# Kernel optimization log

Hardware: AMD Instinct MI355X
Metric: run time of the kernel (lower is better)

## Reference

```python
import jax, jax.numpy as jnp
import numpy as np

DT = 0.04  # CFG.dt in the original repo (Euler step for FitzHugh-Nagumo)


def _fhn_scan(z, dt):
    """Integrate FitzHugh-Nagumo dynamics over time.
    z: (B, T, N) input current per timestep. Returns V: (B, T, N), with V[:,0]=0.
    V[k] = (1+dt)V[k-1] - dt/3 V[k-1]^3 - dt S[k-1] + dt z[k-1]
    S[k] = S[k-1] + dt*0.08*(V[k-1] + 0.7 - 0.8 S[k-1])
    """
    B, T, N = z.shape
    z_t = jnp.transpose(z, (1, 0, 2))  # (T, B, N), time-major for scan

    def step(carry, z_prev):
        V, S = carry
        Vn = (1.0 + dt) * V - (dt / 3.0) * (V ** 3) - dt * S + dt * z_prev
        Sn = S + dt * 0.08 * (V + 0.7 - 0.8 * S)
        return (Vn, Sn), Vn

    init = (jnp.zeros((B, N), z.dtype), jnp.zeros((B, N), z.dtype))
    _, Vs = jax.lax.scan(step, init, z_t[:-1])  # (T-1, B, N): V[1:]
    V = jnp.concatenate([jnp.zeros((1, B, N), z.dtype), Vs], axis=0)
    return jnp.transpose(V, (1, 0, 2))  # (B, T, N)


def setup_inputs() -> dict:
    key = jax.random.key(0)
    k1, k2, k3 = jax.random.split(key, 3)
    B, T = 64, 2048
    batch = jax.random.normal(k1, (B, T, 784), dtype=jnp.float32)
    # nn.Linear default init: U(-1/sqrt(fan_in), 1/sqrt(fan_in))
    W1 = jax.random.uniform(k2, (100, 784), jnp.float32, -1.0, 1.0) / np.sqrt(784.0)
    W2 = jax.random.uniform(k3, (10, 100), jnp.float32, -1.0, 1.0) / np.sqrt(100.0)
    return {"batch": batch, "W1": W1, "W2": W2}


def reference(batch, W1, W2):
    dt = DT
    z1 = jnp.einsum('btd,nd->btn', batch, W1)  # (B, T, 100)
    V1 = _fhn_scan(z1, dt)                      # (B, T, 100)
    z2 = jnp.einsum('btn,mn->btm', V1 * 0.5, W2)  # (B, T, 10)
    V2 = _fhn_scan(z2, dt)                      # (B, T, 10)
    return V2
```

## Files before the change

kernel.cpp:

```cpp
#include <hip/hip_runtime.h>
#include <hip/hip_bf16.h>


#define FHN_DT 0.04f

typedef _Float16 f16x8 __attribute__((ext_vector_type(8)));
typedef __attribute__((ext_vector_type(4))) float          f32x4;
typedef __attribute__((ext_vector_type(8))) unsigned short ushort8;

__device__ __forceinline__ void sync_lds() {
    asm volatile("s_waitcnt lgkmcnt(0)" ::: "memory");
    __builtin_amdgcn_s_barrier();
    asm volatile("" ::: "memory");
}

__global__ void prep_w3(const float* __restrict__ W1, unsigned short* __restrict__ Wg) {
    int idx = blockIdx.x * 256 + threadIdx.x;
    if (idx >= 224000) return;
    int sh    = idx % 40;
    int rest  = idx / 40;
    int n     = rest % 112;
    int rest2 = rest / 112;
    int term  = rest2 % 2;
    int kt    = rest2 / 2;
    int k = kt * 32 + sh;
    float v = (n < 100 && sh < 32 && k < 784) ? W1[n * 784 + k] : 0.0f;
    _Float16 h = (_Float16)v;
    _Float16 l = (_Float16)((v - (float)h) * 1024.0f);
    Wg[idx] = (term == 0) ? __builtin_bit_cast(unsigned short, h)
                          : __builtin_bit_cast(unsigned short, l);
}

#define GW_TILE 8960

__global__ __launch_bounds__(256, 2) void gemm1_n(const float* __restrict__ A,
                                                  const unsigned short* __restrict__ Wg,
                                                  float* __restrict__ z1p) {
    __shared__ __align__(16) unsigned short Wl[2][GW_TILE];
    const int tid  = threadIdx.x;
    const int w    = tid >> 6;
    const int lane = tid & 63;
    const int ln   = lane & 15;
    const int kg   = lane >> 4;
    const long row0 = (long)blockIdx.x * 128;

    const float* arow0 = A + (row0 + w * 32 + ln) * 784 + kg * 8;
    const float* arow1 = arow0 + (size_t)16 * 784;

    f32x4 acc1[2][7] = {};
    f32x4 acc2[2][7] = {};
    float afpA[16], afpB[16];
    ushort8 wreg[5];

#define ISSUE_A(T, AF) {                                                        \
        if ((T) == 24 && kg >= 2) {                                             \
            *(float4*)&AF[0]  = make_float4(0.f, 0.f, 0.f, 0.f);                \
            *(float4*)&AF[4]  = make_float4(0.f, 0.f, 0.f, 0.f);                \
            *(float4*)&AF[8]  = make_float4(0.f, 0.f, 0.f, 0.f);                \
            *(float4*)&AF[12] = make_float4(0.f, 0.f, 0.f, 0.f);                \
        } else {                                                                \
            *(float4*)&AF[0]  = *(const float4*)(arow0 + (T) * 32);             \
            *(float4*)&AF[4]  = *(const float4*)(arow0 + (T) * 32 + 4);         \
            *(float4*)&AF[8]  = *(const float4*)(arow1 + (T) * 32);             \
            *(float4*)&AF[12] = *(const float4*)(arow1 + (T) * 32 + 4);         \
        } }

#define LOADW(T) {                                                              \
        _Pragma("unroll")                                                       \
        for (int j_ = 0; j_ < 5; ++j_) {                                        \
            int off_ = j_ * 4096 + tid * 16;                                    \
            if (off_ < 17920)                                                   \
                wreg[j_] = *(const ushort8*)((const char*)Wg                    \
                            + (size_t)(T) * 17920 + off_);                      \
        } }

#define BODY(KT, AF) {                                                          \
        f16x8 ah0, al0, ah1, al1;                                               \
        _Pragma("unroll")                                                       \
        for (int e_ = 0; e_ < 8; ++e_) {                                        \
            float a0_ = AF[e_], a1_ = AF[8 + e_];                               \
            _Float16 h0_ = (_Float16)a0_, h1_ = (_Float16)a1_;                  \
            ah0[e_] = h0_; ah1[e_] = h1_;                                       \
            al0[e_] = (_Float16)((a0_ - (float)h0_) * 1024.0f);                 \
            al1[e_] = (_Float16)((a1_ - (float)h1_) * 1024.0f);                 \
        }                                                                       \
        {                                                                       \
            unsigned short* buf_ = &Wl[(KT) & 1][0];                            \
            _Pragma("unroll")                                                   \
            for (int j_ = 0; j_ < 5; ++j_) {                                    \
                int off_ = j_ * 4096 + tid * 16;                                \
                if (off_ < 17920) *(ushort8*)((char*)buf_ + off_) = wreg[j_];   \
            }                                                                   \
        }                                                                       \
        if ((KT) < 24) LOADW((KT) + 1);                                         \
        if ((KT) < 23) ISSUE_A((KT) + 2, AF);                                   \
        sync_lds();                                                             \
        const unsigned short* cb_ = &Wl[(KT) & 1][0];                           \
        _Pragma("unroll")                                                       \
        for (int ct_ = 0; ct_ < 7; ++ct_) {                                     \
            const unsigned short* pw_ = cb_ + (ct_ * 16 + ln) * 40 + kg * 8;    \
            f16x8 bh = *(const f16x8*)(pw_);                                    \
            f16x8 bl = *(const f16x8*)(pw_ + 4480);                             \
            acc1[0][ct_] = __builtin_amdgcn_mfma_f32_16x16x32_f16(ah0, bh, acc1[0][ct_], 0, 0, 0); \
            acc2[0][ct_] = __builtin_amdgcn_mfma_f32_16x16x32_f16(ah0, bl, acc2[0][ct_], 0, 0, 0); \
            acc2[0][ct_] = __builtin_amdgcn_mfma_f32_16x16x32_f16(al0, bh, acc2[0][ct_], 0, 0, 0); \
            acc1[1][ct_] = __builtin_amdgcn_mfma_f32_16x16x32_f16(ah1, bh, acc1[1][ct_], 0, 0, 0); \
            acc2[1][ct_] = __builtin_amdgcn_mfma_f32_16x16x32_f16(ah1, bl, acc2[1][ct_], 0, 0, 0); \
            acc2[1][ct_] = __builtin_amdgcn_mfma_f32_16x16x32_f16(al1, bh, acc2[1][ct_], 0, 0, 0); \
        } }

    LOADW(0);
    ISSUE_A(0, afpA);
    ISSUE_A(1, afpB);

    for (int kt2 = 0; kt2 < 12; ++kt2) {
        BODY(kt2 * 2,     afpA);
        BODY(kt2 * 2 + 1, afpB);
    }
    BODY(24, afpA);

#pragma unroll
    for (int ct = 0; ct < 7; ++ct) {
        int n = ct * 16 + ln;
        if (n < 100) {
#pragma unroll
            for (int rt = 0; rt < 2; ++rt) {
                long rg = row0 + w * 32 + rt * 16 + kg * 4;
                float* p = z1p + rg * 100 + n;
#pragma unroll
                for (int r = 0; r < 4; ++r)
                    p[r * 100] = fmaf(acc2[rt][ct][r], 0.0009765625f, acc1[rt][ct][r]);
            }
        }
    }
#undef ISSUE_A
#undef LOADW
#undef BODY
}

__global__ __launch_bounds__(576) void fused_scan3(const float* __restrict__ z1p,
                                                   const float* __restrict__ W2,
                                                   float* __restrict__ out) {
    __shared__ float fsm[32768];
    const int tid = threadIdx.x;
    const int b   = blockIdx.x;
    const float dt = FHN_DT;

    float V = 0.f, S = 0.f;
    const float* zb = z1p + (long)b * 2048 * 100 + tid;
    float z0[16], z1r[16], z2r[16], z3r[16];
    if (tid < 100) {
#pragma unroll
        for (int u = 0; u < 16; ++u) {
            z0[u]  = zb[u * 100];
            z1r[u] = zb[(16 + u) * 100];
            z2r[u] = zb[(32 + u) * 100];
            z3r[u] = zb[(48 + u) * 100];
        }
    }

    const int tg = tid - 128;
    int pp = (tg >> 7) & 3;
    pp = __builtin_amdgcn_readfirstlane(pp);
    const int r  = tg & 127;
    const int mb = (pp == 0) ? 0 : (pp == 1 ? 4 : 7);
    const int mc = (pp == 0) ? 4 : 3;
    const int m2 = tid - 512;

    for (int i = 0; i <= 18; ++i) {
        if (tid < 128) {
            bool a1 = (tid < 100) && (i < 16);
            if (a1) {
#pragma unroll
                for (int sub = 0; sub < 8; ++sub) {
                    float zt[16];
                    int tn = (i * 8 + sub + 4) * 16;
                    if (tn < 2048) {
#pragma unroll
                        for (int u = 0; u < 16; ++u) zt[u] = zb[(tn + u) * 100];
                    }
                    const int cw = i & 1;
#pragma unroll
                    for (int u = 0; u < 16; ++u) {
                        int tl = sub * 16 + u;
                        fsm[cw * 14848 + tl * 116 + tid] = V;
                        float z  = z0[u];
                        float V3 = V * V * V;
                        float Vn = fmaf(1.f + dt, V,
                                    fmaf(-dt / 3.f, V3, fmaf(-dt, S, dt * z)));
                        float Sn = fmaf(dt * 0.08f, V + 0.7f - 0.8f * S, S);
                        V = Vn; S = Sn;
                    }
#pragma unroll
                    for (int u = 0; u < 16; ++u) {
                        z0[u] = z1r[u]; z1r[u] = z2r[u]; z2r[u] = z3r[u]; z3r[u] = zt[u];
                    }
                }
            }
        } else if (tid < 512) {
            if (i >= 1 && i <= 16) {
                const int pb = (i - 1) & 1;
                float acc[4] = {0.f, 0.f, 0.f, 0.f};
                for (int kq = 0; kq < 25; ++kq) {
                    float4 v = *(const float4*)&fsm[pb * 14848 + r * 116 + kq * 4];
#pragma unroll
                    for (int j = 0; j < 4; ++j) {
                        if (j < mc) {
                            const float* wp = W2 + (mb + j) * 100 + kq * 4;
                            acc[j] = fmaf(v.x, wp[0], acc[j]);
                            acc[j] = fmaf(v.y, wp[1], acc[j]);
                            acc[j] = fmaf(v.z, wp[2], acc[j]);
                            acc[j] = fmaf(v.w, wp[3], acc[j]);
                        }
                    }
                }
#pragma unroll
                for (int j = 0; j < 4; ++j)
                    if (j < mc) fsm[29696 + pb * 1536 + r * 12 + mb + j] = 0.5f * acc[j];
            }
            if (i >= 3) {
                const int pb = (i - 1) & 1;
                float* dst = out + ((long)b * 2048 + (long)(i - 3) * 128 + r) * 10;
#pragma unroll
                for (int j = 0; j < 4; ++j)
                    if (j < mc) dst[mb + j] = fsm[pb * 14848 + r * 116 + 100 + mb + j];
            }
        } else {
            bool a2 = (m2 < 10) && (i >= 2) && (i < 18);
            if (a2) {
                const int cw = i & 1;
#pragma unroll
                for (int sub = 0; sub < 8; ++sub) {
                    float z0s[16];
#pragma unroll
                    for (int u = 0; u < 16; ++u)
                        z0s[u] = fsm[29696 + cw * 1536 + (sub * 16 + u) * 12 + m2];
#pragma unroll
                    for (int u = 0; u < 16; ++u) {
                        int tl = sub * 16 + u;
                        fsm[cw * 14848 + tl * 116 + 100 + m2] = V;
                        float z  = z0s[u];
                        float V3 = V * V * V;
                        float Vn = fmaf(1.f + dt, V,
                                    fmaf(-dt / 3.f, V3, fmaf(-dt, S, dt * z)));
                        float Sn = fmaf(dt * 0.08f, V + 0.7f - 0.8f * S, S);
                        V = Vn; S = Sn;
                    }
                }
            }
        }
        sync_lds();
    }
}

extern "C" void kernel_launch(void* const* d_in, const int* in_sizes, int n_in,
                              void* d_out, int out_size, void* d_ws, size_t ws_size,
                              hipStream_t stream) {
    const float* batch = (const float*)d_in[0];
    const float* W1    = (const float*)d_in[1];
    const float* W2    = (const float*)d_in[2];
    float* out = (float*)d_out;

    char* base = (char*)d_ws;
    unsigned short* Wg = (unsigned short*)base;
    float* z1p = (float*)(base + 448000);

    prep_w3<<<875, 256, 0, stream>>>(W1, Wg);
    gemm1_n<<<1024, 256, 0, stream>>>(batch, Wg, z1p);
    fused_scan3<<<64, 576, 0, stream>>>(z1p, W2, out);
}
```

Before: 204.3 us.

## Stage W1 tiles in large LDS sections via direct global-to-LDS loads

```diff
diff --git a/kernel.cpp b/kernel.cpp
--- a/kernel.cpp
+++ b/kernel.cpp
@@ -5,8 +5,13 @@
 #define FHN_DT 0.04f
 
 typedef _Float16 f16x8 __attribute__((ext_vector_type(8)));
-typedef __attribute__((ext_vector_type(4))) float          f32x4;
-typedef __attribute__((ext_vector_type(8))) unsigned short ushort8;
+typedef __attribute__((ext_vector_type(4))) float f32x4;
+
+__device__ __forceinline__ void gl16(const void* g, void* l) {
+    __builtin_amdgcn_global_load_lds(
+        (const __attribute__((address_space(1))) unsigned int*)g,
+        (__attribute__((address_space(3))) unsigned int*)l, 16, 0, 0);
+}
 
 __device__ __forceinline__ void sync_lds() {
     asm volatile("s_waitcnt lgkmcnt(0)" ::: "memory");
@@ -14,35 +19,36 @@
     asm volatile("" ::: "memory");
 }
 
-__global__ void prep_w3(const float* __restrict__ W1, unsigned short* __restrict__ Wg) {
+__global__ void prep_w16(const float* __restrict__ W1, unsigned short* __restrict__ Wg) {
     int idx = blockIdx.x * 256 + threadIdx.x;
-    if (idx >= 224000) return;
-    int sh    = idx % 40;
-    int rest  = idx / 40;
-    int n     = rest % 112;
-    int rest2 = rest / 112;
-    int term  = rest2 % 2;
-    int kt    = rest2 / 2;
-    int k = kt * 32 + sh;
-    float v = (n < 100 && sh < 32 && k < 784) ? W1[n * 784 + k] : 0.0f;
+    if (idx >= 179200) return;
+    int kt   = idx / 7168;
+    int rem  = idx % 7168;
+    int f    = rem >> 9;
+    int r2   = rem & 511;
+    int l    = r2 >> 3;
+    int e    = r2 & 7;
+    int term = f / 7, ct = f % 7;
+    int n = ct * 16 + (l & 15);
+    int k = kt * 32 + (l >> 4) * 8 + e;
+    float v = (n < 100 && k < 784) ? W1[n * 784 + k] : 0.0f;
     _Float16 h = (_Float16)v;
-    _Float16 l = (_Float16)((v - (float)h) * 1024.0f);
-    Wg[idx] = (term == 0) ? __builtin_bit_cast(unsigned short, h)
-                          : __builtin_bit_cast(unsigned short, l);
-}
-
-#define GW_TILE 8960
-
-__global__ __launch_bounds__(256, 2) void gemm1_n(const float* __restrict__ A,
+    unsigned short o;
+    if (term == 0) o = __builtin_bit_cast(unsigned short, h);
+    else           o = __builtin_bit_cast(unsigned short, (_Float16)((v - (float)h) * 1024.0f));
+    Wg[idx] = o;
+}
+
+__global__ __launch_bounds__(512, 1) void gemm1_w(const float* __restrict__ A,
                                                   const unsigned short* __restrict__ Wg,
                                                   float* __restrict__ z1p) {
-    __shared__ __align__(16) unsigned short Wl[2][GW_TILE];
+    __shared__ __align__(16) char smem[129024];
     const int tid  = threadIdx.x;
     const int w    = tid >> 6;
     const int lane = tid & 63;
     const int ln   = lane & 15;
     const int kg   = lane >> 4;
-    const long row0 = (long)blockIdx.x * 128;
+    const long row0 = (long)blockIdx.x * 256;
 
     const float* arow0 = A + (row0 + w * 32 + ln) * 784 + kg * 8;
     const float* arow1 = arow0 + (size_t)16 * 784;
@@ -50,7 +56,6 @@
     f32x4 acc1[2][7] = {};
     f32x4 acc2[2][7] = {};
     float afpA[16], afpB[16];
-    ushort8 wreg[5];
 
 #define ISSUE_A(T, AF) {                                                        \
         if ((T) == 24 && kg >= 2) {                                             \
@@ -65,16 +70,23 @@
             *(float4*)&AF[12] = *(const float4*)(arow1 + (T) * 32 + 4);         \
         } }
 
-#define LOADW(T) {                                                              \
-        _Pragma("unroll")                                                       \
-        for (int j_ = 0; j_ < 5; ++j_) {                                        \
-            int off_ = j_ * 4096 + tid * 16;                                    \
-            if (off_ < 17920)                                                   \
-                wreg[j_] = *(const ushort8*)((const char*)Wg                    \
-                            + (size_t)(T) * 17920 + off_);                      \
-        } }
-
-#define BODY(KT, AF) {                                                          \
+#define LOADSEC(TS, NB) {                                                       \
+        const char* src_ = (const char*)Wg + (size_t)(TS) * 14336;              \
+        _Pragma("unroll 1")                                                     \
+        for (int c_ = 0; c_ < (NB) / 8192; ++c_)                                \
+            gl16(src_ + c_ * 8192 + tid * 16, smem + c_ * 8192 + tid * 16);     \
+        if (((NB) & 8191) != 0 && tid * 16 < ((NB) & 8191))                     \
+            gl16(src_ + ((NB) / 8192) * 8192 + tid * 16,                        \
+                 smem + ((NB) / 8192) * 8192 + tid * 16);                       \
+    }
+
+#define SEC_SYNC() {                                                            \
+        asm volatile("s_waitcnt vmcnt(0)" ::: "memory");                        \
+        __builtin_amdgcn_s_barrier();                                           \
+        asm volatile("" ::: "memory");                                          \
+    }
+
+#define BODY(KT, AF, TS) {                                                      \
         f16x8 ah0, al0, ah1, al1;                                               \
         _Pragma("unroll")                                                       \
         for (int e_ = 0; e_ < 8; ++e_) {                                        \
@@ -84,23 +96,12 @@
             al0[e_] = (_Float16)((a0_ - (float)h0_) * 1024.0f);                 \
             al1[e_] = (_Float16)((a1_ - (float)h1_) * 1024.0f);                 \
         }                                                                       \
-        {                                                                       \
-            unsigned short* buf_ = &Wl[(KT) & 1][0];                            \
-            _Pragma("unroll")                                                   \
-            for (int j_ = 0; j_ < 5; ++j_) {                                    \
-                int off_ = j_ * 4096 + tid * 16;                                \
-                if (off_ < 17920) *(ushort8*)((char*)buf_ + off_) = wreg[j_];   \
-            }                                                                   \
-        }                                                                       \
-        if ((KT) < 24) LOADW((KT) + 1);                                         \
         if ((KT) < 23) ISSUE_A((KT) + 2, AF);                                   \
-        sync_lds();                                                             \
-        const unsigned short* cb_ = &Wl[(KT) & 1][0];                           \
+        const char* cb_ = smem + ((KT) - (TS)) * 14336 + lane * 16;             \
         _Pragma("unroll")                                                       \
         for (int ct_ = 0; ct_ < 7; ++ct_) {                                     \
-            const unsigned short* pw_ = cb_ + (ct_ * 16 + ln) * 40 + kg * 8;    \
-            f16x8 bh = *(const f16x8*)(pw_);                                    \
-            f16x8 bl = *(const f16x8*)(pw_ + 4480);                             \
+            f16x8 bh = *(const f16x8*)(cb_ + ct_ * 1024);                       \
+            f16x8 bl = *(const f16x8*)(cb_ + 7168 + ct_ * 1024);                \
             acc1[0][ct_] = __builtin_amdgcn_mfma_f32_16x16x32_f16(ah0, bh, acc1[0][ct_], 0, 0, 0); \
             acc2[0][ct_] = __builtin_amdgcn_mfma_f32_16x16x32_f16(ah0, bl, acc2[0][ct_], 0, 0, 0); \
             acc2[0][ct_] = __builtin_amdgcn_mfma_f32_16x16x32_f16(al0, bh, acc2[0][ct_], 0, 0, 0); \
@@ -109,15 +110,30 @@
             acc2[1][ct_] = __builtin_amdgcn_mfma_f32_16x16x32_f16(al1, bh, acc2[1][ct_], 0, 0, 0); \
         } }
 
-    LOADW(0);
     ISSUE_A(0, afpA);
     ISSUE_A(1, afpB);
 
-    for (int kt2 = 0; kt2 < 12; ++kt2) {
-        BODY(kt2 * 2,     afpA);
-        BODY(kt2 * 2 + 1, afpB);
-    }
-    BODY(24, afpA);
+    LOADSEC(0, 129024);
+    SEC_SYNC();
+#pragma unroll 1
+    for (int k0 = 0; k0 < 8; k0 += 2) { BODY(k0, afpA, 0); BODY(k0 + 1, afpB, 0); }
+    BODY(8, afpA, 0);
+
+    asm volatile("" ::: "memory");
+    __builtin_amdgcn_s_barrier();
+    asm volatile("" ::: "memory");
+    LOADSEC(9, 114688);
+    SEC_SYNC();
+#pragma unroll 1
+    for (int k0 = 9; k0 < 17; k0 += 2) { BODY(k0, afpB, 9); BODY(k0 + 1, afpA, 9); }
+
+    asm volatile("" ::: "memory");
+    __builtin_amdgcn_s_barrier();
+    asm volatile("" ::: "memory");
+    LOADSEC(17, 114688);
+    SEC_SYNC();
+#pragma unroll 1
+    for (int k0 = 17; k0 < 25; k0 += 2) { BODY(k0, afpB, 17); BODY(k0 + 1, afpA, 17); }
 
 #pragma unroll
     for (int ct = 0; ct < 7; ++ct) {
@@ -134,7 +150,8 @@
         }
     }
 #undef ISSUE_A
-#undef LOADW
+#undef LOADSEC
+#undef SEC_SYNC
 #undef BODY
 }
 
@@ -263,9 +280,9 @@
 
     char* base = (char*)d_ws;
     unsigned short* Wg = (unsigned short*)base;
-    float* z1p = (float*)(base + 448000);
-
-    prep_w3<<<875, 256, 0, stream>>>(W1, Wg);
-    gemm1_n<<<1024, 256, 0, stream>>>(batch, Wg, z1p);
+    float* z1p = (float*)(base + 358400);
+
+    prep_w16<<<700, 256, 0, stream>>>(W1, Wg);
+    gemm1_w<<<512, 512, 0, stream>>>(batch, Wg, z1p);
     fused_scan3<<<64, 576, 0, stream>>>(z1p, W2, out);
 }
```

Result: faster. 188.7 us (-7.6%).
